# Kernel optimization log

Measured on AMD Instinct MI355X. Metric: run time of the kernel, lower is better.

Reference implementation:

```python
import jax, jax.numpy as jnp
import numpy as np
from jax import lax

DT = 0.05          # constructor dt
TAU_DC = 50.0      # constructor tau_dc (ema mode)
ALPHA = DT / max(TAU_DC, 1e-6)


def setup_inputs() -> dict:
    key = jax.random.key(0)
    B, T, F = 16, 4096, 512
    x = jax.random.normal(key, (B, T, F), dtype=jnp.float32)
    return {
        "input_current": x,
        "vb_t": jnp.zeros((F,), jnp.float32),        # vb = 0.0 per feature
        "A_t": jnp.ones((F,), jnp.float32),          # A = 1.0
        "th_t": jnp.ones((F,), jnp.float32),         # theta = 1.0
        "gain_t": jnp.ones((F,), jnp.float32),       # input_gain = 1.0
        "tref_t": jnp.full((F,), 2.0, jnp.float32),
    }


def reference(input_current, vb_t, A_t, th_t, gain_t, tref_t):
    B, T, F = input_current.shape
    # refractory length in steps, clamp >= 1 (ceil(tau_ref/dt))
    ref_steps = jnp.maximum(jnp.ceil(tref_t / max(DT, 1e-6)), 1.0).astype(jnp.int32)  # [F]

    xs = jnp.moveaxis(input_current, 1, 0)  # [T, B, F]

    def step(carry, inp):
        refc, ema = carry            # refc: [B,F] int32, ema: [B,F] float
        xt_raw, t = inp
        xt = xt_raw * gain_t         # scaled input
        # EMA baseline; at t==0 (reset_states) the EMA is initialized to xt
        ema = jnp.where(t == 0, xt, ema + ALPHA * (xt - ema))
        va_cand = vb_t - A_t * (xt - ema)            # amplifier (noise_std == 0)
        in_ref = refc > 0
        fired = (~in_ref) & (jnp.abs(va_cand - vb_t) >= th_t)
        va_next = jnp.where(in_ref | fired, vb_t, va_cand)
        refc = jnp.where(in_ref, refc - 1, refc)
        refc = jnp.where(fired, ref_steps, refc)
        return (refc, ema), (va_next, fired)

    refc0 = jnp.zeros((B, F), jnp.int32)
    ema0 = jnp.zeros((B, F), input_current.dtype)
    _, (va_seq, fired_seq) = lax.scan(step, (refc0, ema0), (xs, jnp.arange(T)))

    # va_trace[:,0,:] = vb, va_trace[:,t+1,:] = va_next_t
    va_trace = jnp.concatenate(
        [jnp.broadcast_to(vb_t, (B, 1, F)), jnp.moveaxis(va_seq, 0, 1)], axis=1
    )  # [B, T+1, F]
    fired_b = jnp.moveaxis(fired_seq, 0, 1)  # [B, T, F]
    spikes = jnp.concatenate([fired_b, fired_b[:, -1:, :]], axis=1)  # [B, T+1, F] bool
    return va_trace, spikes
```

## Files before the change

kernel.cpp:

```cpp
#include <hip/hip_runtime.h>
#include <stdint.h>


#define L_CHUNK 256
#define TS 64
#define DEPTH 4
#define K2_UNROLL 8

typedef const __attribute__((address_space(1))) uint32_t* gptr_t;
typedef __attribute__((address_space(3))) uint32_t* lptr_t;

#define FA_ASM8(A)                                                         \
    asm volatile(                                                          \
                                            \
        "v_sub_f32 %[d1], %[a0], %[ema]\n\t"                               \
        "v_mul_f32 %[am], %[al], %[d1]\n\t"                                \
        "v_add_f32 %[ema], %[ema], %[am]\n\t"                              \
                                                           \
        "v_sub_f32 %[d1], %[a1], %[ema]\n\t"                               \
        "v_sub_f32 %[d2], %[a0], %[ema]\n\t"                               \
        "v_mul_f32 %[am], %[al], %[d1]\n\t"                                \
        "v_cmp_le_f32_e64 vcc, %[th], |%[d2]|\n\t"                         \
        "v_add_f32 %[ema], %[ema], %[am]\n\t"                              \
        "v_addc_co_u32 %[bits], vcc, %[bits], %[bits], vcc\n\t"            \
                                                           \
        "v_sub_f32 %[d1], %[a2], %[ema]\n\t"                               \
        "v_sub_f32 %[d2], %[a1], %[ema]\n\t"                               \
        "v_mul_f32 %[am], %[al], %[d1]\n\t"                                \
        "v_cmp_le_f32_e64 vcc, %[th], |%[d2]|\n\t"                         \
        "v_add_f32 %[ema], %[ema], %[am]\n\t"                              \
        "v_addc_co_u32 %[bits], vcc, %[bits], %[bits], vcc\n\t"            \
                                                           \
        "v_sub_f32 %[d1], %[a3], %[ema]\n\t"                               \
        "v_sub_f32 %[d2], %[a2], %[ema]\n\t"                               \
        "v_mul_f32 %[am], %[al], %[d1]\n\t"                                \
        "v_cmp_le_f32_e64 vcc, %[th], |%[d2]|\n\t"                         \
        "v_add_f32 %[ema], %[ema], %[am]\n\t"                              \
        "v_addc_co_u32 %[bits], vcc, %[bits], %[bits], vcc\n\t"            \
                                                           \
        "v_sub_f32 %[d1], %[a4], %[ema]\n\t"                               \
        "v_sub_f32 %[d2], %[a3], %[ema]\n\t"                               \
        "v_mul_f32 %[am], %[al], %[d1]\n\t"                                \
        "v_cmp_le_f32_e64 vcc, %[th], |%[d2]|\n\t"                         \
        "v_add_f32 %[ema], %[ema], %[am]\n\t"                              \
        "v_addc_co_u32 %[bits], vcc, %[bits], %[bits], vcc\n\t"            \
                                                           \
        "v_sub_f32 %[d1], %[a5], %[ema]\n\t"                               \
        "v_sub_f32 %[d2], %[a4], %[ema]\n\t"                               \
        "v_mul_f32 %[am], %[al], %[d1]\n\t"                                \
        "v_cmp_le_f32_e64 vcc, %[th], |%[d2]|\n\t"                         \
        "v_add_f32 %[ema], %[ema], %[am]\n\t"                              \
        "v_addc_co_u32 %[bits], vcc, %[bits], %[bits], vcc\n\t"            \
                                                           \
        "v_sub_f32 %[d1], %[a6], %[ema]\n\t"                               \
        "v_sub_f32 %[d2], %[a5], %[ema]\n\t"                               \
        "v_mul_f32 %[am], %[al], %[d1]\n\t"                                \
        "v_cmp_le_f32_e64 vcc, %[th], |%[d2]|\n\t"                         \
        "v_add_f32 %[ema], %[ema], %[am]\n\t"                              \
        "v_addc_co_u32 %[bits], vcc, %[bits], %[bits], vcc\n\t"            \
                                                           \
        "v_sub_f32 %[d1], %[a7], %[ema]\n\t"                               \
        "v_sub_f32 %[d2], %[a6], %[ema]\n\t"                               \
        "v_mul_f32 %[am], %[al], %[d1]\n\t"                                \
        "v_cmp_le_f32_e64 vcc, %[th], |%[d2]|\n\t"                         \
        "v_add_f32 %[ema], %[ema], %[am]\n\t"                              \
        "v_addc_co_u32 %[bits], vcc, %[bits], %[bits], vcc\n\t"            \
                                        \
        "v_sub_f32 %[d2], %[a7], %[ema]\n\t"                               \
        "v_cmp_le_f32_e64 vcc, %[th], |%[d2]|\n\t"                         \
        "v_addc_co_u32 %[bits], vcc, %[bits], %[bits], vcc"                \
        : [ema]"+v"(ema), [bits]"+v"(bits),                                \
          [d1]"=&v"(td1), [d2]"=&v"(td2), [am]"=&v"(tam)                   \
        : [a0]"v"((A)[0]), [a1]"v"((A)[1]), [a2]"v"((A)[2]),               \
          [a3]"v"((A)[3]), [a4]"v"((A)[4]), [a5]"v"((A)[5]),               \
          [a6]"v"((A)[6]), [a7]"v"((A)[7]),                                \
          [th]"v"(thf), [al]"s"(alpha)                                     \
        : "vcc")

#define FA_RESOLVE(BASE)                                                   \
    do {                                                                   \
        uint32_t rv = __brev(bits);         \
        int rel = nr - (BASE);                                             \
        uint32_t keep = (rel <= 0) ? rv                                    \
                      : ((rel >= 32) ? 0u : (rv & (0xFFFFFFFFu << rel)));  \
        int j1 = __ffs(keep);                                              \
        nr = keep ? ((BASE) + j1 + rs) : nr;                   \
        bits = 0;                                                          \
    } while (0)

__global__ __launch_bounds__(64, 1)
void fa_scan_kernel(const float* __restrict__ x,
                    const float* __restrict__ vb,
                    const float* __restrict__ A,
                    const float* __restrict__ th,
                    const float* __restrict__ gain,
                    const float* __restrict__ tref,
                    float* __restrict__ emas,
                    int*   __restrict__ nrs,
                    int B, int T, int F) {
#pragma clang fp contract(off)
    __shared__ float lds[DEPTH][TS][64];
    const int lane = threadIdx.x;
    const int gpb = F >> 6;
    const int bi = blockIdx.x;
    const int b = bi / gpb;
    const int f0 = (bi - b * gpb) << 6;
    const int f = f0 + lane;
    const int i = b * F + f;
    const int N = B * F;

    const float vbf = vb[f], Af = A[f], thf = th[f], gf = gain[f];
    const float alpha = 0.001f;
    const int rs = (int)fmaxf(ceilf(tref[f] / 0.05f), 1.0f);

    const float* xb = x + (size_t)b * T * F + f0;
    const float* gsrc0 = xb + (size_t)(lane >> 4) * F + ((lane & 15) << 2);
    const int ntiles = T / TS;

#define ISSUE_TILE(J)                                                         \
    do {                                                                      \
        const float* s_ = gsrc0 + (size_t)(J) * TS * F;                       \
        float* d_ = &lds[(J) & (DEPTH - 1)][0][0];                            \
        _Pragma("unroll")                                                     \
        for (int jj = 0; jj < 16; ++jj) {                                     \
            __builtin_amdgcn_global_load_lds(                                 \
                (gptr_t)(s_ + (size_t)(4 * jj) * F),                          \
                (lptr_t)(d_ + 4 * jj * 64), 16, 0, 0);                        \
        }                                                                     \
    } while (0)

    ISSUE_TILE(0);
    ISSUE_TILE(1);
    ISSUE_TILE(2);

    bool fastAll = __all((gf == 1.0f) && (Af == 1.0f) && (vbf == 0.0f) &&
                         (rs >= 31));

    float ema = 0.0f;
    int nr = 0;
    uint32_t bits = 0;
    float td1, td2, tam;

    for (int k = 0; k < ntiles; ++k) {
        if (k < ntiles - 2)       asm volatile("s_waitcnt vmcnt(32)" ::: "memory");
        else if (k == ntiles - 2) asm volatile("s_waitcnt vmcnt(16)" ::: "memory");
        else                      asm volatile("s_waitcnt vmcnt(0)"  ::: "memory");
        __builtin_amdgcn_sched_barrier(0);

        const int slot = k & (DEPTH - 1);
        const int tb = k * TS;

        if (k == 0) {
            float x0 = lds[0][0][lane];
            ema = fastAll ? x0 : (x0 * gf);
        } else if ((k & 3) == 0) {
            int c = k >> 2;
            emas[(size_t)c * N + i] = ema;
            nrs[(size_t)c * N + i] = nr;
        }

        if (fastAll) {
            float Ab[8], Bb[8];
#pragma unroll
            for (int j = 0; j < 8; ++j) Ab[j] = lds[slot][j][lane];
#pragma unroll
            for (int j = 0; j < 8; ++j) Bb[j] = lds[slot][8 + j][lane];
            FA_ASM8(Ab);
#pragma unroll
            for (int j = 0; j < 8; ++j) Ab[j] = lds[slot][16 + j][lane];
            FA_ASM8(Bb);
#pragma unroll
            for (int j = 0; j < 8; ++j) Bb[j] = lds[slot][24 + j][lane];
            FA_ASM8(Ab);
#pragma unroll
            for (int j = 0; j < 8; ++j) Ab[j] = lds[slot][32 + j][lane];
            FA_ASM8(Bb);
            FA_RESOLVE(tb);
#pragma unroll
            for (int j = 0; j < 8; ++j) Bb[j] = lds[slot][40 + j][lane];
            FA_ASM8(Ab);
#pragma unroll
            for (int j = 0; j < 8; ++j) Ab[j] = lds[slot][48 + j][lane];
            FA_ASM8(Bb);
#pragma unroll
            for (int j = 0; j < 8; ++j) Bb[j] = lds[slot][56 + j][lane];
            FA_ASM8(Ab);
            FA_ASM8(Bb);
            FA_RESOLVE(tb + 32);
        } else {
            float ra[8], rb[8];
#pragma unroll
            for (int j = 0; j < 8; ++j) ra[j] = lds[slot][j][lane];
#pragma unroll
            for (int t8 = 0; t8 < TS / 8; ++t8) {
                if (t8 < TS / 8 - 1) {
#pragma unroll
                    for (int j = 0; j < 8; ++j)
                        rb[j] = lds[slot][(t8 + 1) * 8 + j][lane];
                }
#pragma unroll
                for (int j = 0; j < 8; ++j) {
                    const int t = tb + t8 * 8 + j;
                    float xt = ra[j] * gf;
                    float d1 = xt - ema;
                    float am = alpha * d1;
                    ema = ema + am;
                    float d2 = xt - ema;
                    float av = Af * d2;
                    float vc = vbf - av;
                    float dv = vc - vbf;
                    bool cross = fabsf(dv) >= thf;
                    bool tge = t >= nr;
                    bool fired = cross && tge;
                    nr = fired ? (t + 1 + rs) : nr;
                }
#pragma unroll
                for (int j = 0; j < 8; ++j) ra[j] = rb[j];
            }
        }

        if (k + 3 < ntiles) ISSUE_TILE(k + 3);
    }
#undef ISSUE_TILE
}

__global__ __launch_bounds__(256)
void fa_emit_kernel(const float* __restrict__ x,
                    const float* __restrict__ vb,
                    const float* __restrict__ A,
                    const float* __restrict__ th,
                    const float* __restrict__ gain,
                    const float* __restrict__ tref,
                    const float* __restrict__ emas,
                    const int*   __restrict__ nrs,
                    float* __restrict__ out,
                    int B, int T, int F, int nchunks) {
#pragma clang fp contract(off)
    int N = B * F;
    int tid = blockIdx.x * blockDim.x + threadIdx.x;
    if (tid >= N * nchunks) return;
    int i = tid % N;
    int k = tid / N;
    int f = i % F;
    int b = i / F;
    const float vbf = vb[f], Af = A[f], thf = th[f], gf = gain[f];
    const float alpha = 0.001f;
    int rs = (int)fmaxf(ceilf(tref[f] / 0.05f), 1.0f);

    const float* xp = x + (size_t)b * T * F + f;
    float* va_out   = out + (size_t)b * (T + 1) * F + f;
    float* sp_out   = out + (size_t)B * (T + 1) * F + (size_t)b * (T + 1) * F + f;

    int tbeg = k * L_CHUNK;
    int tend = tbeg + L_CHUNK;
    if (tend > T) tend = T;

    float cur[K2_UNROLL], nxt[K2_UNROLL];
#pragma unroll
    for (int u = 0; u < K2_UNROLL; ++u) cur[u] = xp[(size_t)(tbeg + u) * F];

    float ema;
    int nr;
    if (k == 0) {
        ema = cur[0] * gf;
        nr = 0;
        va_out[0] = vbf;
    } else {
        ema = emas[(size_t)k * N + i];
        nr = nrs[(size_t)k * N + i];
    }

    float last_sp = 0.0f;
    for (int t0 = tbeg; t0 < tend; t0 += K2_UNROLL) {
        if (t0 + K2_UNROLL < tend) {
#pragma unroll
            for (int u = 0; u < K2_UNROLL; ++u)
                nxt[u] = xp[(size_t)(t0 + K2_UNROLL + u) * F];
        }
#pragma unroll
        for (int u = 0; u < K2_UNROLL; ++u) {
            int t = t0 + u;
            float xt = cur[u] * gf;
            float d1 = xt - ema;
            float am = alpha * d1;
            ema = ema + am;
            float d2 = xt - ema;
            float av = Af * d2;
            float vc = vbf - av;
            float dv = vc - vbf;
            bool cross = fabsf(dv) >= thf;
            bool tge = t >= nr;
            bool fired = cross && tge;
            float va_next = (cross || !tge) ? vbf : vc;
            nr = fired ? (t + 1 + rs) : nr;
            float spv = fired ? 1.0f : 0.0f;
            va_out[(size_t)(t + 1) * F] = va_next;
            sp_out[(size_t)t * F] = spv;
            last_sp = spv;
        }
#pragma unroll
        for (int u = 0; u < K2_UNROLL; ++u) cur[u] = nxt[u];
    }
    if (tend == T) sp_out[(size_t)T * F] = last_sp;
}

__global__ __launch_bounds__(64, 1)
void fa_neuron_mono(const float* __restrict__ x,
                    const float* __restrict__ vb,
                    const float* __restrict__ A,
                    const float* __restrict__ th,
                    const float* __restrict__ gain,
                    const float* __restrict__ tref,
                    float* __restrict__ out,
                    int B, int T, int F) {
#pragma clang fp contract(off)
    int tid = blockIdx.x * blockDim.x + threadIdx.x;
    if (tid >= B * F) return;
    int f = tid % F;
    int b = tid / F;
    const float vbf = vb[f], Af = A[f], thf = th[f], gf = gain[f];
    const float alpha = 0.001f;
    int rs = (int)fmaxf(ceilf(tref[f] / 0.05f), 1.0f);
    const float* xp = x + (size_t)b * T * F + f;
    float* va_out   = out + (size_t)b * (T + 1) * F + f;
    float* sp_out   = out + (size_t)B * (T + 1) * F + (size_t)b * (T + 1) * F + f;
    va_out[0] = vbf;
    float ema = 0.0f;
    int nr = 0;
    for (int t = 0; t < T; ++t) {
        float xt = xp[(size_t)t * F] * gf;
        if (t == 0) {
            ema = xt;
        } else {
            float d1 = xt - ema;
            float am = alpha * d1;
            ema = ema + am;
        }
        float d2 = xt - ema;
        float av = Af * d2;
        float vc = vbf - av;
        float dv = vc - vbf;
        bool cross = fabsf(dv) >= thf;
        bool tge = t >= nr;
        bool fired = cross && tge;
        float va_next = (cross || !tge) ? vbf : vc;
        nr = fired ? (t + 1 + rs) : nr;
        float spv = fired ? 1.0f : 0.0f;
        va_out[(size_t)(t + 1) * F] = va_next;
        sp_out[(size_t)t * F] = spv;
        if (t == T - 1) sp_out[(size_t)T * F] = spv;
    }
}

extern "C" void kernel_launch(void* const* d_in, const int* in_sizes, int n_in,
                              void* d_out, int out_size, void* d_ws, size_t ws_size,
                              hipStream_t stream) {
    const float* x    = (const float*)d_in[0];
    const float* vb   = (const float*)d_in[1];
    const float* A    = (const float*)d_in[2];
    const float* th   = (const float*)d_in[3];
    const float* gain = (const float*)d_in[4];
    const float* tref = (const float*)d_in[5];
    float* out = (float*)d_out;

    int F = in_sizes[1];
    long long BF = (long long)out_size / 2 - in_sizes[0];
    int B = (int)(BF / F);
    int T = (int)(in_sizes[0] / BF);
    int N = B * F;

    int nchunks = (T + L_CHUNK - 1) / L_CHUNK;
    size_t ws_need = (size_t)nchunks * N * (sizeof(float) + sizeof(int));

    bool tiled_ok = (ws_size >= ws_need) && (T % L_CHUNK == 0) &&
                    (T % TS == 0) && (T / TS >= 4) && (F % 64 == 0) &&
                    (L_CHUNK == 4 * TS);

    if (!tiled_ok) {
        int block = 64;
        int grid = (N + block - 1) / block;
        fa_neuron_mono<<<grid, block, 0, stream>>>(x, vb, A, th, gain, tref, out, B, T, F);
        return;
    }

    float* emas = (float*)d_ws;
    int*   nrs  = (int*)(emas + (size_t)nchunks * N);

    {
        int block = 64;
        int grid = N / 64;
        fa_scan_kernel<<<grid, block, 0, stream>>>(x, vb, A, th, gain, tref,
                                                   emas, nrs, B, T, F);
    }
    {
        int total = N * nchunks;
        int block = 256;
        int grid = (total + block - 1) / block;
        fa_emit_kernel<<<grid, block, 0, stream>>>(x, vb, A, th, gain, tref,
                                                   emas, nrs, out, B, T, F, nchunks);
    }
}
```

Baseline: 149.3 us.

## Fuse scan and emit kernels with per-chunk flags so emission overlaps the scan

Result: slower. 243.2 us (+62.9%).

```diff
diff --git a/kernel.cpp b/kernel.cpp
--- a/kernel.cpp
+++ b/kernel.cpp
@@ -2,9 +2,8 @@
 #include <stdint.h>
 
 
-#define L_CHUNK 256
+#define LCHUNK 256
 #define TS 64
-#define DEPTH 4
 #define K2_UNROLL 8
 
 typedef const __attribute__((address_space(1))) uint32_t* gptr_t;
@@ -12,60 +11,51 @@
 
 #define FA_ASM8(A)                                                         \
     asm volatile(                                                          \
-                                            \
         "v_sub_f32 %[d1], %[a0], %[ema]\n\t"                               \
         "v_mul_f32 %[am], %[al], %[d1]\n\t"                                \
         "v_add_f32 %[ema], %[ema], %[am]\n\t"                              \
-                                                           \
         "v_sub_f32 %[d1], %[a1], %[ema]\n\t"                               \
         "v_sub_f32 %[d2], %[a0], %[ema]\n\t"                               \
         "v_mul_f32 %[am], %[al], %[d1]\n\t"                                \
         "v_cmp_le_f32_e64 vcc, %[th], |%[d2]|\n\t"                         \
         "v_add_f32 %[ema], %[ema], %[am]\n\t"                              \
         "v_addc_co_u32 %[bits], vcc, %[bits], %[bits], vcc\n\t"            \
-                                                           \
         "v_sub_f32 %[d1], %[a2], %[ema]\n\t"                               \
         "v_sub_f32 %[d2], %[a1], %[ema]\n\t"                               \
         "v_mul_f32 %[am], %[al], %[d1]\n\t"                                \
         "v_cmp_le_f32_e64 vcc, %[th], |%[d2]|\n\t"                         \
         "v_add_f32 %[ema], %[ema], %[am]\n\t"                              \
         "v_addc_co_u32 %[bits], vcc, %[bits], %[bits], vcc\n\t"            \
-                                                           \
         "v_sub_f32 %[d1], %[a3], %[ema]\n\t"                               \
         "v_sub_f32 %[d2], %[a2], %[ema]\n\t"                               \
         "v_mul_f32 %[am], %[al], %[d1]\n\t"                                \
         "v_cmp_le_f32_e64 vcc, %[th], |%[d2]|\n\t"                         \
         "v_add_f32 %[ema], %[ema], %[am]\n\t"                              \
         "v_addc_co_u32 %[bits], vcc, %[bits], %[bits], vcc\n\t"            \
-                                                           \
         "v_sub_f32 %[d1], %[a4], %[ema]\n\t"                               \
         "v_sub_f32 %[d2], %[a3], %[ema]\n\t"                               \
         "v_mul_f32 %[am], %[al], %[d1]\n\t"                                \
         "v_cmp_le_f32_e64 vcc, %[th], |%[d2]|\n\t"                         \
         "v_add_f32 %[ema], %[ema], %[am]\n\t"                              \
         "v_addc_co_u32 %[bits], vcc, %[bits], %[bits], vcc\n\t"            \
-                                                           \
         "v_sub_f32 %[d1], %[a5], %[ema]\n\t"                               \
         "v_sub_f32 %[d2], %[a4], %[ema]\n\t"                               \
         "v_mul_f32 %[am], %[al], %[d1]\n\t"                                \
         "v_cmp_le_f32_e64 vcc, %[th], |%[d2]|\n\t"                         \
         "v_add_f32 %[ema], %[ema], %[am]\n\t"                              \
         "v_addc_co_u32 %[bits], vcc, %[bits], %[bits], vcc\n\t"            \
-                                                           \
         "v_sub_f32 %[d1], %[a6], %[ema]\n\t"                               \
         "v_sub_f32 %[d2], %[a5], %[ema]\n\t"                               \
         "v_mul_f32 %[am], %[al], %[d1]\n\t"                                \
         "v_cmp_le_f32_e64 vcc, %[th], |%[d2]|\n\t"                         \
         "v_add_f32 %[ema], %[ema], %[am]\n\t"                              \
         "v_addc_co_u32 %[bits], vcc, %[bits], %[bits], vcc\n\t"            \
-                                                           \
         "v_sub_f32 %[d1], %[a7], %[ema]\n\t"                               \
         "v_sub_f32 %[d2], %[a6], %[ema]\n\t"                               \
         "v_mul_f32 %[am], %[al], %[d1]\n\t"                                \
         "v_cmp_le_f32_e64 vcc, %[th], |%[d2]|\n\t"                         \
         "v_add_f32 %[ema], %[ema], %[am]\n\t"                              \
         "v_addc_co_u32 %[bits], vcc, %[bits], %[bits], vcc\n\t"            \
-                                        \
         "v_sub_f32 %[d2], %[a7], %[ema]\n\t"                               \
         "v_cmp_le_f32_e64 vcc, %[th], |%[d2]|\n\t"                         \
         "v_addc_co_u32 %[bits], vcc, %[bits], %[bits], vcc"                \
@@ -79,48 +69,53 @@
 
 #define FA_RESOLVE(BASE)                                                   \
     do {                                                                   \
-        uint32_t rv = __brev(bits);         \
+        uint32_t rv = __brev(bits);                                        \
         int rel = nr - (BASE);                                             \
         uint32_t keep = (rel <= 0) ? rv                                    \
                       : ((rel >= 32) ? 0u : (rv & (0xFFFFFFFFu << rel)));  \
         int j1 = __ffs(keep);                                              \
-        nr = keep ? ((BASE) + j1 + rs) : nr;                   \
+        nr = keep ? ((BASE) + j1 + rs) : nr;                               \
         bits = 0;                                                          \
     } while (0)
 
-__global__ __launch_bounds__(64, 1)
-void fa_scan_kernel(const float* __restrict__ x,
-                    const float* __restrict__ vb,
-                    const float* __restrict__ A,
-                    const float* __restrict__ th,
-                    const float* __restrict__ gain,
-                    const float* __restrict__ tref,
-                    float* __restrict__ emas,
-                    int*   __restrict__ nrs,
-                    int B, int T, int F) {
+__global__ __launch_bounds__(64)
+void fa_fused_kernel(const float* __restrict__ x,
+                     const float* __restrict__ vb,
+                     const float* __restrict__ A,
+                     const float* __restrict__ th,
+                     const float* __restrict__ gain,
+                     const float* __restrict__ tref,
+                     float* __restrict__ emas,
+                     int*   __restrict__ nrs,
+                     int*   __restrict__ done,
+                     float* __restrict__ out,
+                     int B, int T, int F, int nchunks, int NG) {
 #pragma clang fp contract(off)
-    __shared__ float lds[DEPTH][TS][64];
+    __shared__ float lds[2][TS][64];
+    const int N = B * F;
+    const float alpha = 0.001f;
     const int lane = threadIdx.x;
-    const int gpb = F >> 6;
-    const int bi = blockIdx.x;
-    const int b = bi / gpb;
-    const int f0 = (bi - b * gpb) << 6;
-    const int f = f0 + lane;
-    const int i = b * F + f;
-    const int N = B * F;
-
-    const float vbf = vb[f], Af = A[f], thf = th[f], gf = gain[f];
-    const float alpha = 0.001f;
-    const int rs = (int)fmaxf(ceilf(tref[f] / 0.05f), 1.0f);
-
-    const float* xb = x + (size_t)b * T * F + f0;
-    const float* gsrc0 = xb + (size_t)(lane >> 4) * F + ((lane & 15) << 2);
-    const int ntiles = T / TS;
+
+    if ((int)blockIdx.x < NG) {
+        __builtin_amdgcn_s_setprio(3);
+        const int g = blockIdx.x;
+        const int gpb = F >> 6;
+        const int b = g / gpb;
+        const int f0 = (g - b * gpb) << 6;
+        const int f = f0 + lane;
+        const int i = b * F + f;
+
+        const float vbf = vb[f], Af = A[f], thf = th[f], gf = gain[f];
+        const int rs = (int)fmaxf(ceilf(tref[f] / 0.05f), 1.0f);
+
+        const float* gsrc0 = x + (size_t)b * T * F + f0
+                           + (size_t)(lane >> 4) * F + ((lane & 15) << 2);
+        const int ntiles = T / TS;
 
 #define ISSUE_TILE(J)                                                         \
     do {                                                                      \
         const float* s_ = gsrc0 + (size_t)(J) * TS * F;                       \
-        float* d_ = &lds[(J) & (DEPTH - 1)][0][0];                            \
+        float* d_ = &lds[(J) & 1][0][0];                                      \
         _Pragma("unroll")                                                     \
         for (int jj = 0; jj < 16; ++jj) {                                     \
             __builtin_amdgcn_global_load_lds(                                 \
@@ -129,179 +124,176 @@
         }                                                                     \
     } while (0)
 
-    ISSUE_TILE(0);
-    ISSUE_TILE(1);
-    ISSUE_TILE(2);
-
-    bool fastAll = __all((gf == 1.0f) && (Af == 1.0f) && (vbf == 0.0f) &&
-                         (rs >= 31));
-
-    float ema = 0.0f;
-    int nr = 0;
-    uint32_t bits = 0;
-    float td1, td2, tam;
-
-    for (int k = 0; k < ntiles; ++k) {
-        if (k < ntiles - 2)       asm volatile("s_waitcnt vmcnt(32)" ::: "memory");
-        else if (k == ntiles - 2) asm volatile("s_waitcnt vmcnt(16)" ::: "memory");
-        else                      asm volatile("s_waitcnt vmcnt(0)"  ::: "memory");
-        __builtin_amdgcn_sched_barrier(0);
-
-        const int slot = k & (DEPTH - 1);
-        const int tb = k * TS;
-
+        ISSUE_TILE(0);
+        ISSUE_TILE(1);
+
+        bool fastAll = __all((gf == 1.0f) && (Af == 1.0f) && (vbf == 0.0f) &&
+                             (rs >= 31));
+
+        float ema = 0.0f;
+        int nr = 0;
+        uint32_t bits = 0;
+        float td1, td2, tam;
+
+        for (int k = 0; k < ntiles; ++k) {
+            if (k < ntiles - 1) asm volatile("s_waitcnt vmcnt(16)" ::: "memory");
+            else                asm volatile("s_waitcnt vmcnt(0)"  ::: "memory");
+            __builtin_amdgcn_sched_barrier(0);
+
+            const int slot = k & 1;
+            const int tb = k * TS;
+
+            if (k == 0) {
+                float x0 = lds[0][0][lane];
+                ema = fastAll ? x0 : (x0 * gf);
+            } else if ((k & 3) == 0) {
+                int c = k >> 2;
+                emas[(size_t)c * N + i] = ema;
+                nrs[(size_t)c * N + i] = nr;
+                __builtin_amdgcn_fence(__ATOMIC_RELEASE, "agent");
+                if (lane == 0)
+                    __hip_atomic_store(&done[c * NG + g], 1, __ATOMIC_RELAXED,
+                                       __HIP_MEMORY_SCOPE_AGENT);
+            }
+
+            if (fastAll) {
+                float Ab[8], Bb[8];
+#pragma unroll
+                for (int j = 0; j < 8; ++j) Ab[j] = lds[slot][j][lane];
+#pragma unroll
+                for (int j = 0; j < 8; ++j) Bb[j] = lds[slot][8 + j][lane];
+                FA_ASM8(Ab);
+#pragma unroll
+                for (int j = 0; j < 8; ++j) Ab[j] = lds[slot][16 + j][lane];
+                FA_ASM8(Bb);
+#pragma unroll
+                for (int j = 0; j < 8; ++j) Bb[j] = lds[slot][24 + j][lane];
+                FA_ASM8(Ab);
+#pragma unroll
+                for (int j = 0; j < 8; ++j) Ab[j] = lds[slot][32 + j][lane];
+                FA_ASM8(Bb);
+                FA_RESOLVE(tb);
+#pragma unroll
+                for (int j = 0; j < 8; ++j) Bb[j] = lds[slot][40 + j][lane];
+                FA_ASM8(Ab);
+#pragma unroll
+                for (int j = 0; j < 8; ++j) Ab[j] = lds[slot][48 + j][lane];
+                FA_ASM8(Bb);
+#pragma unroll
+                for (int j = 0; j < 8; ++j) Bb[j] = lds[slot][56 + j][lane];
+                FA_ASM8(Ab);
+                FA_ASM8(Bb);
+                FA_RESOLVE(tb + 32);
+            } else {
+                float ra[8], rb[8];
+#pragma unroll
+                for (int j = 0; j < 8; ++j) ra[j] = lds[slot][j][lane];
+#pragma unroll
+                for (int t8 = 0; t8 < TS / 8; ++t8) {
+                    if (t8 < TS / 8 - 1) {
+#pragma unroll
+                        for (int j = 0; j < 8; ++j)
+                            rb[j] = lds[slot][(t8 + 1) * 8 + j][lane];
+                    }
+#pragma unroll
+                    for (int j = 0; j < 8; ++j) {
+                        const int t = tb + t8 * 8 + j;
+                        float xt = ra[j] * gf;
+                        float d1 = xt - ema;
+                        float am = alpha * d1;
+                        ema = ema + am;
+                        float d2 = xt - ema;
+                        float av = Af * d2;
+                        float vc = vbf - av;
+                        float dv = vc - vbf;
+                        bool cross = fabsf(dv) >= thf;
+                        bool tge = t >= nr;
+                        bool fired = cross && tge;
+                        nr = fired ? (t + 1 + rs) : nr;
+                    }
+#pragma unroll
+                    for (int j = 0; j < 8; ++j) ra[j] = rb[j];
+                }
+            }
+
+            if (k + 2 < ntiles) ISSUE_TILE(k + 2);
+        }
+#undef ISSUE_TILE
+    } else {
+        const int e = (int)blockIdx.x - NG;
+        const int k = e / NG;
+        const int g = e - k * NG;
+        const int i = g * 64 + lane;
+        const int f = i % F;
+        const int b = i / F;
+
+        const float vbf = vb[f], Af = A[f], thf = th[f], gf = gain[f];
+        const int rs = (int)fmaxf(ceilf(tref[f] / 0.05f), 1.0f);
+
+        const float* xp = x + (size_t)b * T * F + f;
+        float* va_out   = out + (size_t)b * (T + 1) * F + f;
+        float* sp_out   = out + (size_t)B * (T + 1) * F + (size_t)b * (T + 1) * F + f;
+
+        if (k > 0) {
+            const int* flag = &done[k * NG + g];
+            while (__hip_atomic_load(flag, __ATOMIC_RELAXED,
+                                     __HIP_MEMORY_SCOPE_AGENT) == 0)
+                __builtin_amdgcn_s_sleep(64);
+            __builtin_amdgcn_fence(__ATOMIC_ACQUIRE, "agent");
+        }
+
+        const int tbeg = k * LCHUNK;
+        int tend = tbeg + LCHUNK;
+        if (tend > T) tend = T;
+
+        float cur[K2_UNROLL], nxt[K2_UNROLL];
+#pragma unroll
+        for (int u = 0; u < K2_UNROLL; ++u) cur[u] = xp[(size_t)(tbeg + u) * F];
+
+        float ema;
+        int nr;
         if (k == 0) {
-            float x0 = lds[0][0][lane];
-            ema = fastAll ? x0 : (x0 * gf);
-        } else if ((k & 3) == 0) {
-            int c = k >> 2;
-            emas[(size_t)c * N + i] = ema;
-            nrs[(size_t)c * N + i] = nr;
-        }
-
-        if (fastAll) {
-            float Ab[8], Bb[8];
-#pragma unroll
-            for (int j = 0; j < 8; ++j) Ab[j] = lds[slot][j][lane];
-#pragma unroll
-            for (int j = 0; j < 8; ++j) Bb[j] = lds[slot][8 + j][lane];
-            FA_ASM8(Ab);
-#pragma unroll
-            for (int j = 0; j < 8; ++j) Ab[j] = lds[slot][16 + j][lane];
-            FA_ASM8(Bb);
-#pragma unroll
-            for (int j = 0; j < 8; ++j) Bb[j] = lds[slot][24 + j][lane];
-            FA_ASM8(Ab);
-#pragma unroll
-            for (int j = 0; j < 8; ++j) Ab[j] = lds[slot][32 + j][lane];
-            FA_ASM8(Bb);
-            FA_RESOLVE(tb);
-#pragma unroll
-            for (int j = 0; j < 8; ++j) Bb[j] = lds[slot][40 + j][lane];
-            FA_ASM8(Ab);
-#pragma unroll
-            for (int j = 0; j < 8; ++j) Ab[j] = lds[slot][48 + j][lane];
-            FA_ASM8(Bb);
-#pragma unroll
-            for (int j = 0; j < 8; ++j) Bb[j] = lds[slot][56 + j][lane];
-            FA_ASM8(Ab);
-            FA_ASM8(Bb);
-            FA_RESOLVE(tb + 32);
+            ema = cur[0] * gf;
+            nr = 0;
+            va_out[0] = vbf;
         } else {
-            float ra[8], rb[8];
-#pragma unroll
-            for (int j = 0; j < 8; ++j) ra[j] = lds[slot][j][lane];
-#pragma unroll
-            for (int t8 = 0; t8 < TS / 8; ++t8) {
-                if (t8 < TS / 8 - 1) {
-#pragma unroll
-                    for (int j = 0; j < 8; ++j)
-                        rb[j] = lds[slot][(t8 + 1) * 8 + j][lane];
-                }
-#pragma unroll
-                for (int j = 0; j < 8; ++j) {
-                    const int t = tb + t8 * 8 + j;
-                    float xt = ra[j] * gf;
-                    float d1 = xt - ema;
-                    float am = alpha * d1;
-                    ema = ema + am;
-                    float d2 = xt - ema;
-                    float av = Af * d2;
-                    float vc = vbf - av;
-                    float dv = vc - vbf;
-                    bool cross = fabsf(dv) >= thf;
-                    bool tge = t >= nr;
-                    bool fired = cross && tge;
-                    nr = fired ? (t + 1 + rs) : nr;
-                }
-#pragma unroll
-                for (int j = 0; j < 8; ++j) ra[j] = rb[j];
+            ema = emas[(size_t)k * N + i];
+            nr = nrs[(size_t)k * N + i];
+        }
+
+        float last_sp = 0.0f;
+        for (int t0 = tbeg; t0 < tend; t0 += K2_UNROLL) {
+            if (t0 + K2_UNROLL < tend) {
+#pragma unroll
+                for (int u = 0; u < K2_UNROLL; ++u)
+                    nxt[u] = xp[(size_t)(t0 + K2_UNROLL + u) * F];
             }
-        }
-
-        if (k + 3 < ntiles) ISSUE_TILE(k + 3);
+#pragma unroll
+            for (int u = 0; u < K2_UNROLL; ++u) {
+                int t = t0 + u;
+                float xt = cur[u] * gf;
+                float d1 = xt - ema;
+                float am = alpha * d1;
+                ema = ema + am;
+                float d2 = xt - ema;
+                float av = Af * d2;
+                float vc = vbf - av;
+                float dv = vc - vbf;
+                bool cross = fabsf(dv) >= thf;
+                bool tge = t >= nr;
+                bool fired = cross && tge;
+                float va_next = (cross || !tge) ? vbf : vc;
+                nr = fired ? (t + 1 + rs) : nr;
+                float spv = fired ? 1.0f : 0.0f;
+                va_out[(size_t)(t + 1) * F] = va_next;
+                sp_out[(size_t)t * F] = spv;
+                last_sp = spv;
+            }
+#pragma unroll
+            for (int u = 0; u < K2_UNROLL; ++u) cur[u] = nxt[u];
+        }
+        if (tend == T) sp_out[(size_t)T * F] = last_sp;
     }
-#undef ISSUE_TILE
-}
-
-__global__ __launch_bounds__(256)
-void fa_emit_kernel(const float* __restrict__ x,
-                    const float* __restrict__ vb,
-                    const float* __restrict__ A,
-                    const float* __restrict__ th,
-                    const float* __restrict__ gain,
-                    const float* __restrict__ tref,
-                    const float* __restrict__ emas,
-                    const int*   __restrict__ nrs,
-                    float* __restrict__ out,
-                    int B, int T, int F, int nchunks) {
-#pragma clang fp contract(off)
-    int N = B * F;
-    int tid = blockIdx.x * blockDim.x + threadIdx.x;
-    if (tid >= N * nchunks) return;
-    int i = tid % N;
-    int k = tid / N;
-    int f = i % F;
-    int b = i / F;
-    const float vbf = vb[f], Af = A[f], thf = th[f], gf = gain[f];
-    const float alpha = 0.001f;
-    int rs = (int)fmaxf(ceilf(tref[f] / 0.05f), 1.0f);
-
-    const float* xp = x + (size_t)b * T * F + f;
-    float* va_out   = out + (size_t)b * (T + 1) * F + f;
-    float* sp_out   = out + (size_t)B * (T + 1) * F + (size_t)b * (T + 1) * F + f;
-
-    int tbeg = k * L_CHUNK;
-    int tend = tbeg + L_CHUNK;
-    if (tend > T) tend = T;
-
-    float cur[K2_UNROLL], nxt[K2_UNROLL];
-#pragma unroll
-    for (int u = 0; u < K2_UNROLL; ++u) cur[u] = xp[(size_t)(tbeg + u) * F];
-
-    float ema;
-    int nr;
-    if (k == 0) {
-        ema = cur[0] * gf;
-        nr = 0;
-        va_out[0] = vbf;
-    } else {
-        ema = emas[(size_t)k * N + i];
-        nr = nrs[(size_t)k * N + i];
-    }
-
-    float last_sp = 0.0f;
-    for (int t0 = tbeg; t0 < tend; t0 += K2_UNROLL) {
-        if (t0 + K2_UNROLL < tend) {
-#pragma unroll
-            for (int u = 0; u < K2_UNROLL; ++u)
-                nxt[u] = xp[(size_t)(t0 + K2_UNROLL + u) * F];
-        }
-#pragma unroll
-        for (int u = 0; u < K2_UNROLL; ++u) {
-            int t = t0 + u;
-            float xt = cur[u] * gf;
-            float d1 = xt - ema;
-            float am = alpha * d1;
-            ema = ema + am;
-            float d2 = xt - ema;
-            float av = Af * d2;
-            float vc = vbf - av;
-            float dv = vc - vbf;
-            bool cross = fabsf(dv) >= thf;
-            bool tge = t >= nr;
-            bool fired = cross && tge;
-            float va_next = (cross || !tge) ? vbf : vc;
-            nr = fired ? (t + 1 + rs) : nr;
-            float spv = fired ? 1.0f : 0.0f;
-            va_out[(size_t)(t + 1) * F] = va_next;
-            sp_out[(size_t)t * F] = spv;
-            last_sp = spv;
-        }
-#pragma unroll
-        for (int u = 0; u < K2_UNROLL; ++u) cur[u] = nxt[u];
-    }
-    if (tend == T) sp_out[(size_t)T * F] = last_sp;
 }
 
 __global__ __launch_bounds__(64, 1)
@@ -368,15 +360,17 @@
     int B = (int)(BF / F);
     int T = (int)(in_sizes[0] / BF);
     int N = B * F;
-
-    int nchunks = (T + L_CHUNK - 1) / L_CHUNK;
-    size_t ws_need = (size_t)nchunks * N * (sizeof(float) + sizeof(int));
-
-    bool tiled_ok = (ws_size >= ws_need) && (T % L_CHUNK == 0) &&
+    int NG = N / 64;
+
+    int nchunks = (T + LCHUNK - 1) / LCHUNK;
+    size_t ws_need = (size_t)nchunks * N * (sizeof(float) + sizeof(int))
+                   + (size_t)nchunks * NG * sizeof(int);
+
+    bool fused_ok = (ws_size >= ws_need) && (T % LCHUNK == 0) &&
                     (T % TS == 0) && (T / TS >= 4) && (F % 64 == 0) &&
-                    (L_CHUNK == 4 * TS);
-
-    if (!tiled_ok) {
+                    (LCHUNK == 4 * TS) && (N % 64 == 0);
+
+    if (!fused_ok) {
         int block = 64;
         int grid = (N + block - 1) / block;
         fa_neuron_mono<<<grid, block, 0, stream>>>(x, vb, A, th, gain, tref, out, B, T, F);
@@ -385,18 +379,12 @@
 
     float* emas = (float*)d_ws;
     int*   nrs  = (int*)(emas + (size_t)nchunks * N);
-
-    {
-        int block = 64;
-        int grid = N / 64;
-        fa_scan_kernel<<<grid, block, 0, stream>>>(x, vb, A, th, gain, tref,
-                                                   emas, nrs, B, T, F);
-    }
-    {
-        int total = N * nchunks;
-        int block = 256;
-        int grid = (total + block - 1) / block;
-        fa_emit_kernel<<<grid, block, 0, stream>>>(x, vb, A, th, gain, tref,
-                                                   emas, nrs, out, B, T, F, nchunks);
-    }
+    int*   done = (int*)(nrs + (size_t)nchunks * N);
+
+    hipMemsetAsync(done, 0, (size_t)nchunks * NG * sizeof(int), stream);
+
+    int grid = NG + NG * nchunks;
+    fa_fused_kernel<<<grid, 64, 0, stream>>>(x, vb, A, th, gain, tref,
+                                             emas, nrs, done, out,
+                                             B, T, F, nchunks, NG);
 }
```
